# Optimization experiments

Hardware: AMD Instinct MI355X
Metric: run time of the kernel (lower is better)

The kernel has to match this reference:

```python
import jax, jax.numpy as jnp
import numpy as np

N_EMBED = 1024
N_HEAD = 64  # head (value) dimension, per source: Linear(n_embed, n_head)
B = 8
C = 2048


def setup_inputs() -> dict:
    key = jax.random.key(0)
    k1, k2, k3, k4, k5 = jax.random.split(key, 5)
    bound = 1.0 / np.sqrt(N_EMBED)  # torch Linear default init range
    x = jax.random.normal(k1, (B, C, N_EMBED), dtype=jnp.float32)
    Wq = jax.random.uniform(k2, (N_EMBED, N_HEAD), dtype=jnp.float32, minval=-bound, maxval=bound)
    Wk = jax.random.uniform(k3, (N_EMBED, N_HEAD), dtype=jnp.float32, minval=-bound, maxval=bound)
    Wv = jax.random.uniform(k4, (N_EMBED, N_HEAD), dtype=jnp.float32, minval=-bound, maxval=bound)
    zero_mask = jax.random.randint(k5, (B, C), 0, 2) == 1
    return {"x": x, "Wq": Wq, "Wk": Wk, "Wv": Wv, "zero_mask": zero_mask}


def reference(x, Wq, Wk, Wv, zero_mask):
    # x: [B, C, n_embed]; zero_mask: [B, C] bool (zeroes whole query rows post-softmax)
    Bc, Cc, _ = x.shape
    q = x @ Wq  # [B, C, H]
    k = x @ Wk
    v = x @ Wv
    # NOTE: source scales by C**-0.5 (sequence length), not head_dim**-0.5
    scores = jnp.einsum('bqh,bkh->bqk', q, k) * (float(Cc) ** -0.5)  # [B, C, C]
    causal = jnp.tril(jnp.ones((Cc, Cc), dtype=bool))
    scores = jnp.where(causal[None], scores, -jnp.inf)
    a = jax.nn.softmax(scores, axis=-1)
    a = jnp.where(zero_mask[..., None], jnp.zeros((), dtype=a.dtype), a)  # post-softmax zero mask
    return a @ v  # [B, C, H]
```

## Files before the change

### kernel.cpp

```cpp
#include <hip/hip_runtime.h>
#include <math.h>


#define B_ 8
#define C_ 2048
#define E_ 1024
#define H_ 64
#define SCALE 0.02209708691207961f

typedef __attribute__((ext_vector_type(8))) short short8;
typedef __attribute__((ext_vector_type(4))) float floatx4;

union BF8 { short8 s8; unsigned int u[4]; };

static __device__ __forceinline__ unsigned int pack_bf2(float lo, float hi) {
    unsigned int a = __builtin_bit_cast(unsigned int, lo);
    unsigned int b = __builtin_bit_cast(unsigned int, hi);
    return (a >> 16) | (b & 0xFFFF0000u);
}
static __device__ __forceinline__ unsigned short f2bf(float f) {
    return (unsigned short)(__builtin_bit_cast(unsigned int, f) >> 16);
}
static __device__ __forceinline__ void load_lds16(const void* g, void* l) {
    __builtin_amdgcn_global_load_lds(
        (const __attribute__((address_space(1))) void*)g,
        (__attribute__((address_space(3))) void*)l, 16, 0, 0);
}

__global__ __launch_bounds__(256) void wcvt_kernel(
    const float* __restrict__ Wq, const float* __restrict__ Wk,
    const float* __restrict__ Wv, unsigned short* __restrict__ wt)
{
    __shared__ float lds[64][68];
    const int bid = (int)blockIdx.x;
    const int m = bid >> 4, kt = bid & 15, k0 = kt * 64;
    const float* W = (m == 0) ? Wq : (m == 1) ? Wk : Wv;
    const int t = (int)threadIdx.x;
#pragma unroll
    for (int j = 0; j < 4; j++) {
        int idx4 = j * 256 + t;
        int row = idx4 >> 4, c4 = idx4 & 15;
        float4 v = *(const float4*)(W + (size_t)(k0 + row) * 64 + c4 * 4);
        *(float4*)&lds[row][c4 * 4] = v;
    }
    __syncthreads();
#pragma unroll
    for (int j = 0; j < 2; j++) {
        int g = j * 256 + t;
        int n = g >> 3, kk = (g & 7) * 8;
        unsigned int o[4];
#pragma unroll
        for (int i = 0; i < 4; i++)
            o[i] = pack_bf2(lds[kk + 2 * i][n], lds[kk + 2 * i + 1][n]);
        *(uint4*)(wt + (size_t)(m * 64 + n) * 1024 + k0 + kk) =
            make_uint4(o[0], o[1], o[2], o[3]);
    }
}

__global__ __launch_bounds__(512, 1) void qkv_kernel(
    const float* __restrict__ X, const unsigned short* __restrict__ wt,
    unsigned short* __restrict__ qg, unsigned short* __restrict__ kg,
    unsigned short* __restrict__ vtile)
{
    __shared__ unsigned short wlds[64 * 1032];
    __shared__ unsigned short vstage[64 * 136];

    const int t = (int)threadIdx.x;
    const int w = t >> 6, lane = t & 63;
    const int l15 = lane & 15, quad = lane >> 4;
    const int rt = (int)blockIdx.x, m = (int)blockIdx.y;
    const int r0 = rt * 128;
    const int mrow = r0 + w * 16 + l15;
    const unsigned short* wsrc = wt + (size_t)m * 64 * 1024;

#pragma unroll
    for (int j = 0; j < 16; j++) {
        int idx = j * 512 + t;
        int row = idx >> 7, g = idx & 127;
        uint4 v = *(const uint4*)(wsrc + (size_t)row * 1024 + g * 8);
        *(uint4*)&wlds[row * 1032 + g * 8] = v;
    }

    floatx4 acc[4];
#pragma unroll
    for (int j = 0; j < 4; j++) acc[j] = (floatx4){0.f, 0.f, 0.f, 0.f};

    float4 xb[3][4];
#pragma unroll
    for (int p = 0; p < 2; p++)
#pragma unroll
        for (int kc = 0; kc < 2; kc++) {
            const float* xp = X + (size_t)mrow * E_ + p * 64 + kc * 32 + quad * 8;
            xb[p][kc * 2]     = *(const float4*)xp;
            xb[p][kc * 2 + 1] = *(const float4*)(xp + 4);
        }

    __syncthreads();

#pragma unroll
    for (int c = 0; c < 16; c++) {
        const int cur = c % 3, nxt = (c + 2) % 3;
        if (c + 2 < 16) {
            const int k0n = (c + 2) * 64;
#pragma unroll
            for (int kc = 0; kc < 2; kc++) {
                const float* xp = X + (size_t)mrow * E_ + k0n + kc * 32 + quad * 8;
                xb[nxt][kc * 2]     = *(const float4*)xp;
                xb[nxt][kc * 2 + 1] = *(const float4*)(xp + 4);
            }
        }
#pragma unroll
        for (int ks = 0; ks < 2; ks++) {
            BF8 a;
            float4 f0 = xb[cur][ks * 2], f1 = xb[cur][ks * 2 + 1];
            a.u[0] = pack_bf2(f0.x, f0.y);
            a.u[1] = pack_bf2(f0.z, f0.w);
            a.u[2] = pack_bf2(f1.x, f1.y);
            a.u[3] = pack_bf2(f1.z, f1.w);
#pragma unroll
            for (int nt = 0; nt < 4; nt++) {
                const int n = nt * 16 + l15;
                short8 bfr = *(const short8*)&wlds[n * 1032 + c * 64
                                                  + ks * 32 + quad * 8];
                acc[nt] = __builtin_amdgcn_mfma_f32_16x16x32_bf16(
                    a.s8, bfr, acc[nt], 0, 0, 0);
            }
        }
    }

    const int bb = r0 >> 11;
    const int keybase = r0 & 2047;
    const int rowl = w * 16 + quad * 4;
    if (m == 0) {
#pragma unroll
        for (int nt = 0; nt < 4; nt++)
#pragma unroll
            for (int r = 0; r < 4; r++)
                qg[(size_t)(r0 + rowl + r) * 64 + nt * 16 + l15] =
                    f2bf(acc[nt][r] * SCALE);
    } else if (m == 1) {
#pragma unroll
        for (int nt = 0; nt < 4; nt++)
#pragma unroll
            for (int r = 0; r < 4; r++)
                kg[(size_t)(r0 + rowl + r) * 64 + nt * 16 + l15] =
                    f2bf(acc[nt][r]);
    } else {
#pragma unroll
        for (int nt = 0; nt < 4; nt++) {
            const int h = nt * 16 + l15;
            *(unsigned int*)&vstage[h * 136 + rowl] =
                pack_bf2(acc[nt][0], acc[nt][1]);
            *(unsigned int*)&vstage[h * 136 + rowl + 2] =
                pack_bf2(acc[nt][2], acc[nt][3]);
        }
        __syncthreads();
#pragma unroll
        for (int j = 0; j < 2; j++) {
            int idx = j * 512 + t;
            int h = idx >> 4, g = idx & 15;
            uint4 v = *(const uint4*)&vstage[h * 136 + g * 8];
            int kb = (keybase >> 6) + (g >> 3);
            *(uint4*)(vtile + (((size_t)bb * 32 + kb) * 64 + h) * 64
                      + (g & 7) * 8) = v;
        }
    }
}

__global__ __launch_bounds__(128, 2) void attn_kernel(
    const unsigned short* __restrict__ qg, const unsigned short* __restrict__ kg,
    const unsigned short* __restrict__ vtile, const int* __restrict__ zmask,
    float* __restrict__ opart, float* __restrict__ lpart,
    float* __restrict__ out)
{
    __shared__ unsigned short Klds[2][64 * 64];
    __shared__ unsigned short Vlds[2][64 * 64];
    __shared__ unsigned short Ps[2 * 16 * 88];

    const int t = (int)threadIdx.x;
    const int w = t >> 6, lane = t & 63;
    const int l15 = lane & 15, quad = lane >> 4;
    const int b = (int)blockIdx.x;
    const int qt = (int)blockIdx.y;
    const int z = (int)blockIdx.z;
    const int q0 = qt * 32;
    const int nkt = (q0 >> 6) + 1;
    const int t0 = z * 8;
    const int t1 = (t0 + 8 < nkt) ? (t0 + 8) : nkt;
    if (t0 >= t1) return;
    const int ns = (nkt + 7) >> 3;

    const int qlo = q0 + w * 16;
    const int myrow = qlo + quad * 4;
    const int srow_off = lane >> 3, sgs = lane & 7;

    short8 qfr[2];
#pragma unroll
    for (int kc = 0; kc < 2; kc++)
        qfr[kc] = *(const short8*)(qg + ((size_t)b * C_ + qlo + l15) * 64
                                   + kc * 32 + quad * 8);

    floatx4 accO[4];
#pragma unroll
    for (int i = 0; i < 4; i++) accO[i] = (floatx4){0.f, 0.f, 0.f, 0.f};
    float lsum[4] = {0.f, 0.f, 0.f, 0.f};

#pragma unroll
    for (int j = 0; j < 4; j++) {
        const int region = w * 4 + j;
        const int row = region * 8 + srow_off;
        const int gsrc = sgs ^ (row & 7);
        load_lds16(kg + ((size_t)b * C_ + t0 * 64 + row) * 64 + gsrc * 8,
                   &Klds[0][region * 512]);
        load_lds16(vtile + (((size_t)b * 32 + t0) * 64 + row) * 64 + gsrc * 8,
                   &Vlds[0][region * 512]);
    }

    int buf = 0;
    for (int kt = t0; kt < t1; kt++) {
        __syncthreads();
        if (kt + 1 < t1) {
            const int k0n = (kt + 1) * 64;
#pragma unroll
            for (int j = 0; j < 4; j++) {
                const int region = w * 4 + j;
                const int row = region * 8 + srow_off;
                const int gsrc = sgs ^ (row & 7);
                load_lds16(kg + ((size_t)b * C_ + k0n + row) * 64 + gsrc * 8,
                           &Klds[buf ^ 1][region * 512]);
                load_lds16(vtile + (((size_t)b * 32 + kt + 1) * 64 + row) * 64 + gsrc * 8,
                           &Vlds[buf ^ 1][region * 512]);
            }
        }

        floatx4 s[4];
#pragma unroll
        for (int nt = 0; nt < 4; nt++) {
            const int row = nt * 16 + l15;
            short8 kf0 = *(const short8*)&Klds[buf][row * 64 + ((quad) ^ (row & 7)) * 8];
            short8 kf1 = *(const short8*)&Klds[buf][row * 64 + ((4 + quad) ^ (row & 7)) * 8];
            floatx4 zz = (floatx4){0.f, 0.f, 0.f, 0.f};
            zz = __builtin_amdgcn_mfma_f32_16x16x32_bf16(qfr[0], kf0, zz, 0, 0, 0);
            s[nt] = __builtin_amdgcn_mfma_f32_16x16x32_bf16(qfr[1], kf1, zz, 0, 0, 0);
        }
        float pr[4][4];
#pragma unroll
        for (int nt = 0; nt < 4; nt++)
#pragma unroll
            for (int r = 0; r < 4; r++) pr[nt][r] = __expf(s[nt][r]);
        if (kt == nkt - 1) {
            const int k0 = kt * 64;
#pragma unroll
            for (int nt = 0; nt < 4; nt++) {
                const int key = k0 + nt * 16 + l15;
#pragma unroll
                for (int r = 0; r < 4; r++)
                    if (key > myrow + r) pr[nt][r] = 0.f;
            }
        }
#pragma unroll
        for (int nt = 0; nt < 4; nt++)
#pragma unroll
            for (int r = 0; r < 4; r++) {
                lsum[r] += pr[nt][r];
                Ps[(w * 16 + quad * 4 + r) * 88 + nt * 16 + l15] = f2bf(pr[nt][r]);
            }
#pragma unroll
        for (int kc = 0; kc < 2; kc++) {
            short8 af = *(const short8*)&Ps[(w * 16 + l15) * 88 + kc * 32 + quad * 8];
#pragma unroll
            for (int nt = 0; nt < 4; nt++) {
                const int row = nt * 16 + l15;
                short8 vf = *(const short8*)&Vlds[buf][row * 64
                                + ((kc * 4 + quad) ^ (row & 7)) * 8];
                accO[nt] = __builtin_amdgcn_mfma_f32_16x16x32_bf16(
                    af, vf, accO[nt], 0, 0, 0);
            }
        }
        buf ^= 1;
    }

#pragma unroll
    for (int r = 0; r < 4; r++) {
        float v = lsum[r];
        v += __shfl_xor(v, 1);
        v += __shfl_xor(v, 2);
        v += __shfl_xor(v, 4);
        v += __shfl_xor(v, 8);
        lsum[r] = v;
    }

    if (ns == 1) {
        float inv[4];
#pragma unroll
        for (int r = 0; r < 4; r++) {
            int zm = zmask[b * C_ + myrow + r];
            inv[r] = zm ? 0.f : 1.0f / lsum[r];
        }
#pragma unroll
        for (int nt = 0; nt < 4; nt++)
#pragma unroll
            for (int r = 0; r < 4; r++)
                out[(size_t)(b * C_ + myrow + r) * 64 + nt * 16 + l15] =
                    accO[nt][r] * inv[r];
    } else {
        const int lrow = myrow - 512;
        float* ob = opart + ((size_t)(z * 8 + b) * 1536 + lrow) * 64;
#pragma unroll
        for (int nt = 0; nt < 4; nt++)
#pragma unroll
            for (int r = 0; r < 4; r++)
                ob[(size_t)r * 64 + nt * 16 + l15] = accO[nt][r];
        if (l15 == 0) {
#pragma unroll
            for (int r = 0; r < 4; r++)
                lpart[(size_t)(z * 8 + b) * 1536 + lrow + r] = lsum[r];
        }
    }
}

__global__ __launch_bounds__(256) void combine_kernel(
    const float* __restrict__ opart, const float* __restrict__ lpart,
    const int* __restrict__ zmask, float* __restrict__ out)
{
    const int b = (int)blockIdx.y;
    const int gid = (int)blockIdx.x * 256 + (int)threadIdx.x;
    const int lrow = gid >> 4;
    const int f4 = gid & 15;
    const int row = 512 + lrow;
    const int nkt = (row >> 6) + 1;
    const int ns = (nkt + 7) >> 3;

    float4 o = make_float4(0.f, 0.f, 0.f, 0.f);
    float l = 0.f;
    for (int zc = 0; zc < ns; zc++) {
        float4 p = *(const float4*)(opart
            + ((size_t)(zc * 8 + b) * 1536 + lrow) * 64 + f4 * 4);
        o.x += p.x; o.y += p.y; o.z += p.z; o.w += p.w;
        l += lpart[(size_t)(zc * 8 + b) * 1536 + lrow];
    }
    const float inv = zmask[b * C_ + row] ? 0.f : 1.0f / l;
    *(float4*)(out + (size_t)(b * C_ + row) * 64 + f4 * 4) =
        make_float4(o.x * inv, o.y * inv, o.z * inv, o.w * inv);
}

extern "C" void kernel_launch(void* const* d_in, const int* in_sizes, int n_in,
                              void* d_out, int out_size, void* d_ws, size_t ws_size,
                              hipStream_t stream) {
    const float* X  = (const float*)d_in[0];
    const float* Wq = (const float*)d_in[1];
    const float* Wk = (const float*)d_in[2];
    const float* Wv = (const float*)d_in[3];
    const int*   zm = (const int*)d_in[4];
    float* out = (float*)d_out;

    unsigned short* qg    = (unsigned short*)d_ws;
    unsigned short* kg    = qg    + (size_t)B_ * C_ * H_;
    unsigned short* vtile = kg    + (size_t)B_ * C_ * H_;
    unsigned short* wt    = vtile + (size_t)B_ * C_ * H_;
    float* opart = (float*)(wt + (size_t)192 * 1024);
    float* lpart = opart + (size_t)4 * 8 * 1536 * 64;

    wcvt_kernel<<<dim3(48), dim3(256), 0, stream>>>(Wq, Wk, Wv, wt);
    qkv_kernel<<<dim3(128, 3), dim3(512), 0, stream>>>(X, wt, qg, kg, vtile);
    attn_kernel<<<dim3(B_, 64, 4), dim3(128), 0, stream>>>(
        qg, kg, vtile, zm, opart, lpart, out);
    combine_kernel<<<dim3(96, B_), dim3(256), 0, stream>>>(opart, lpart, zm, out);
}
```

Before: 149.2 us.

## Fuse Q/K/V projections per row tile with async LDS-staged X and W pipeline

```diff
diff --git a/kernel.cpp b/kernel.cpp
--- a/kernel.cpp
+++ b/kernel.cpp
@@ -57,113 +57,116 @@
     }
 }
 
-__global__ __launch_bounds__(512, 1) void qkv_kernel(
+__global__ __launch_bounds__(256, 2) void qkv_kernel(
     const float* __restrict__ X, const unsigned short* __restrict__ wt,
     unsigned short* __restrict__ qg, unsigned short* __restrict__ kg,
     unsigned short* __restrict__ vtile)
 {
-    __shared__ unsigned short wlds[64 * 1032];
-    __shared__ unsigned short vstage[64 * 136];
+    __shared__ __align__(16) unsigned char smem[3 * 8192 + 2 * 24576];
+    unsigned short* vstage = (unsigned short*)smem;
 
     const int t = (int)threadIdx.x;
     const int w = t >> 6, lane = t & 63;
     const int l15 = lane & 15, quad = lane >> 4;
-    const int rt = (int)blockIdx.x, m = (int)blockIdx.y;
-    const int r0 = rt * 128;
-    const int mrow = r0 + w * 16 + l15;
-    const unsigned short* wsrc = wt + (size_t)m * 64 * 1024;
-
-#pragma unroll
-    for (int j = 0; j < 16; j++) {
-        int idx = j * 512 + t;
-        int row = idx >> 7, g = idx & 127;
-        uint4 v = *(const uint4*)(wsrc + (size_t)row * 1024 + g * 8);
-        *(uint4*)&wlds[row * 1032 + g * 8] = v;
-    }
-
-    floatx4 acc[4];
-#pragma unroll
-    for (int j = 0; j < 4; j++) acc[j] = (floatx4){0.f, 0.f, 0.f, 0.f};
-
-    float4 xb[3][4];
-#pragma unroll
-    for (int p = 0; p < 2; p++)
-#pragma unroll
-        for (int kc = 0; kc < 2; kc++) {
-            const float* xp = X + (size_t)mrow * E_ + p * 64 + kc * 32 + quad * 8;
-            xb[p][kc * 2]     = *(const float4*)xp;
-            xb[p][kc * 2 + 1] = *(const float4*)(xp + 4);
-        }
-
-    __syncthreads();
+    const int r0 = (int)blockIdx.x * 32;
+    const int ncol0 = (w & 1) * 96;
+    const int rbase = (w >> 1) * 16;
+
+    const int xgi0 = w * 128 + lane;
+    const int xr_a = xgi0 >> 4, xs_a = xgi0 & 15;
+    const int xg_a = xs_a ^ (xr_a & 15);
+    const int xr_b = (xgi0 + 64) >> 4, xs_b = xgi0 & 15;
+    const int xg_b = xs_b ^ (xr_b & 15);
+    const int wrow_off = lane >> 3, wgs = lane & 7;
+
+    floatx4 acc[6];
+#pragma unroll
+    for (int j = 0; j < 6; j++) acc[j] = (floatx4){0.f, 0.f, 0.f, 0.f};
+
+#define STAGE_X(c, q) do {                                                   \
+        load_lds16(X + (size_t)(r0 + xr_a) * E_ + (c) * 64 + xg_a * 4,       \
+                   smem + (q) * 8192 + (w * 128) * 16);                      \
+        load_lds16(X + (size_t)(r0 + xr_b) * E_ + (c) * 64 + xg_b * 4,       \
+                   smem + (q) * 8192 + (w * 128 + 64) * 16);                 \
+    } while (0)
+#define STAGE_W(c, q) do {                                                   \
+        _Pragma("unroll")                                                    \
+        for (int j = 0; j < 6; j++) {                                        \
+            const int region = w * 6 + j;                                    \
+            const int row = region * 8 + wrow_off;                           \
+            const int gsrc = wgs ^ (row & 7);                                \
+            load_lds16(wt + (size_t)row * 1024 + (c) * 64 + gsrc * 8,        \
+                       smem + 24576 + (q) * 24576 + region * 1024);          \
+        }                                                                    \
+    } while (0)
+
+    STAGE_X(0, 0);
+    STAGE_X(1, 1);
+    STAGE_W(0, 0);
 
 #pragma unroll
     for (int c = 0; c < 16; c++) {
-        const int cur = c % 3, nxt = (c + 2) % 3;
-        if (c + 2 < 16) {
-            const int k0n = (c + 2) * 64;
-#pragma unroll
-            for (int kc = 0; kc < 2; kc++) {
-                const float* xp = X + (size_t)mrow * E_ + k0n + kc * 32 + quad * 8;
-                xb[nxt][kc * 2]     = *(const float4*)xp;
-                xb[nxt][kc * 2 + 1] = *(const float4*)(xp + 4);
-            }
-        }
+        __syncthreads();
+        if (c + 2 < 16) STAGE_X(c + 2, (c + 2) % 3);
+        if (c + 1 < 16) STAGE_W(c + 1, (c + 1) & 1);
+
+        const float4* xc = (const float4*)(smem + (c % 3) * 8192);
+        const unsigned short* wc =
+            (const unsigned short*)(smem + 24576 + (c & 1) * 24576);
+
 #pragma unroll
         for (int ks = 0; ks < 2; ks++) {
+            const int g0 = ks * 8 + quad * 2;
+            const float4* xrow = xc + (rbase + l15) * 16;
+            float4 f0 = xrow[g0 ^ l15];
+            float4 f1 = xrow[(g0 + 1) ^ l15];
             BF8 a;
-            float4 f0 = xb[cur][ks * 2], f1 = xb[cur][ks * 2 + 1];
             a.u[0] = pack_bf2(f0.x, f0.y);
             a.u[1] = pack_bf2(f0.z, f0.w);
             a.u[2] = pack_bf2(f1.x, f1.y);
             a.u[3] = pack_bf2(f1.z, f1.w);
 #pragma unroll
-            for (int nt = 0; nt < 4; nt++) {
-                const int n = nt * 16 + l15;
-                short8 bfr = *(const short8*)&wlds[n * 1032 + c * 64
-                                                  + ks * 32 + quad * 8];
+            for (int nt = 0; nt < 6; nt++) {
+                const int n = ncol0 + nt * 16 + l15;
+                const int slot = (ks * 4 + quad) ^ (n & 7);
+                short8 bfr = *(const short8*)(wc + n * 64 + slot * 8);
                 acc[nt] = __builtin_amdgcn_mfma_f32_16x16x32_bf16(
                     a.s8, bfr, acc[nt], 0, 0, 0);
             }
         }
     }
-
+#undef STAGE_X
+#undef STAGE_W
+
+    __syncthreads();
     const int bb = r0 >> 11;
     const int keybase = r0 & 2047;
-    const int rowl = w * 16 + quad * 4;
-    if (m == 0) {
-#pragma unroll
-        for (int nt = 0; nt < 4; nt++)
-#pragma unroll
-            for (int r = 0; r < 4; r++)
-                qg[(size_t)(r0 + rowl + r) * 64 + nt * 16 + l15] =
-                    f2bf(acc[nt][r] * SCALE);
-    } else if (m == 1) {
-#pragma unroll
-        for (int nt = 0; nt < 4; nt++)
-#pragma unroll
-            for (int r = 0; r < 4; r++)
-                kg[(size_t)(r0 + rowl + r) * 64 + nt * 16 + l15] =
-                    f2bf(acc[nt][r]);
-    } else {
-#pragma unroll
-        for (int nt = 0; nt < 4; nt++) {
-            const int h = nt * 16 + l15;
-            *(unsigned int*)&vstage[h * 136 + rowl] =
+    const int rowl0 = rbase + quad * 4;
+#pragma unroll
+    for (int nt = 0; nt < 6; nt++) {
+        const int n = ncol0 + nt * 16 + l15;
+        if (n < 64) {
+#pragma unroll
+            for (int r = 0; r < 4; r++)
+                qg[(size_t)(r0 + rowl0 + r) * 64 + n] = f2bf(acc[nt][r] * SCALE);
+        } else if (n < 128) {
+#pragma unroll
+            for (int r = 0; r < 4; r++)
+                kg[(size_t)(r0 + rowl0 + r) * 64 + (n - 64)] = f2bf(acc[nt][r]);
+        } else {
+            const int h = n - 128;
+            *(unsigned int*)&vstage[h * 40 + rowl0] =
                 pack_bf2(acc[nt][0], acc[nt][1]);
-            *(unsigned int*)&vstage[h * 136 + rowl + 2] =
+            *(unsigned int*)&vstage[h * 40 + rowl0 + 2] =
                 pack_bf2(acc[nt][2], acc[nt][3]);
         }
-        __syncthreads();
-#pragma unroll
-        for (int j = 0; j < 2; j++) {
-            int idx = j * 512 + t;
-            int h = idx >> 4, g = idx & 15;
-            uint4 v = *(const uint4*)&vstage[h * 136 + g * 8];
-            int kb = (keybase >> 6) + (g >> 3);
-            *(uint4*)(vtile + (((size_t)bb * 32 + kb) * 64 + h) * 64
-                      + (g & 7) * 8) = v;
-        }
+    }
+    __syncthreads();
+    {
+        const int h = t >> 2, part = t & 3;
+        uint4 v = *(const uint4*)&vstage[h * 40 + part * 8];
+        *(uint4*)(vtile + ((size_t)(bb * 32 + (keybase >> 6)) * 64 + h) * 64
+                  + (keybase & 63) + part * 8) = v;
     }
 }
 
@@ -362,7 +365,7 @@
     float* lpart = opart + (size_t)4 * 8 * 1536 * 64;
 
     wcvt_kernel<<<dim3(48), dim3(256), 0, stream>>>(Wq, Wk, Wv, wt);
-    qkv_kernel<<<dim3(128, 3), dim3(512), 0, stream>>>(X, wt, qg, kg, vtile);
+    qkv_kernel<<<dim3(512), dim3(256), 0, stream>>>(X, wt, qg, kg, vtile);
     attn_kernel<<<dim3(B_, 64, 4), dim3(128), 0, stream>>>(
         qg, kg, vtile, zm, opart, lpart, out);
     combine_kernel<<<dim3(96, B_), dim3(256), 0, stream>>>(opart, lpart, zm, out);
```

After: 138.7 us. -7.0%, faster.
